# Optimization experiments

Measured on AMD Instinct MI355X. Metric: run time of the kernel, lower is better.

The kernel has to match this reference:

```python
import jax, jax.numpy as jnp
import numpy as np

HEADS = 4
DIM_HEAD = 128


def setup_inputs() -> dict:
    key = jax.random.key(0)
    k1, k2, k3, k4, k5 = jax.random.split(key, 5)
    dim = 256
    f, h, w = 8, 14, 14
    inner = HEADS * DIM_HEAD
    scale = DIM_HEAD ** -0.5
    fmap = jax.random.normal(k1, (8, dim, f, h, w), dtype=jnp.float32)
    # Conv3d 1x1x1, no bias -> plain channel matmul weight [3*inner, dim]
    W_qkv = jax.random.normal(k2, (3 * inner, dim), dtype=jnp.float32) * (dim ** -0.5)
    pos_f = jax.random.normal(k3, (f, DIM_HEAD), dtype=jnp.float32) * scale
    pos_h = jax.random.normal(k4, (h, DIM_HEAD), dtype=jnp.float32) * scale
    pos_w = jax.random.normal(k5, (w, DIM_HEAD), dtype=jnp.float32) * scale
    return {"fmap": fmap, "W_qkv": W_qkv, "pos_f": pos_f, "pos_h": pos_h, "pos_w": pos_w}


def reference(fmap, W_qkv, pos_f, pos_h, pos_w):
    b, c, f, h, w = fmap.shape
    n = f * h * w
    scale = DIM_HEAD ** -0.5
    # 1x1x1 Conv3d == channel matmul
    qkv = jnp.einsum('bcfhw,oc->bofhw', fmap, W_qkv)  # [b, 3*inner, f, h, w]
    q, k, v = jnp.split(qkv, 3, axis=1)
    # 'b (h d) x y z -> b h (x y z) d'
    def to_heads(t):
        return t.reshape(b, HEADS, DIM_HEAD, n).transpose(0, 1, 3, 2)
    q, k, v = to_heads(q), to_heads(k), to_heads(v)
    q = q * scale
    # additive absolute positional embedding [n, d]
    emb = (pos_f[:, None, None, :] + pos_h[None, :, None, :] + pos_w[None, None, :, :]).reshape(n, DIM_HEAD)
    sim = jnp.einsum('bhid,bhjd->bhij', q, k) + jnp.einsum('bhid,jd->bhij', q, emb)
    attn = jax.nn.softmax(sim, axis=-1)
    out = jnp.einsum('bhij,bhjd->bhid', attn, v)  # [b, heads, n, d]
    # 'b h (x y z) d -> b (h d) x y z'
    out = out.transpose(0, 1, 3, 2).reshape(b, HEADS * DIM_HEAD, f, h, w)
    return out
```

## Files before the change

### kernel.cpp

```cpp
#include <hip/hip_runtime.h>
#include <hip/hip_bf16.h>
#include <cstdint>

#define NPOS 1568
#define NQPAD 1664
#define NKVT 25
#define DHEAD 128
#define DIM 256
#define SCALE_Q (0.08838834764831845f * 1.4426950408889634f)

typedef __bf16 bf16x8 __attribute__((ext_vector_type(8)));
typedef float f32x4 __attribute__((ext_vector_type(4)));
typedef float f32x16 __attribute__((ext_vector_type(16)));
typedef unsigned short u16;
typedef u16 u16x8 __attribute__((ext_vector_type(8)));

__device__ __forceinline__ unsigned cvtpk(float a, float b) {
  unsigned r;
  asm("v_cvt_pk_bf16_f32 %0, %1, %2" : "=v"(r) : "v"(a), "v"(b));
  return r;
}

__device__ __forceinline__ void gload_lds16(const void* g, void* s) {
  __builtin_amdgcn_global_load_lds(
      (const __attribute__((address_space(1))) unsigned*)g,
      (__attribute__((address_space(3))) unsigned*)s, 16, 0, 0);
}

__device__ __forceinline__ f32x16 zero16() {
  f32x16 v;
#pragma unroll
  for (int i = 0; i < 16; ++i) v[i] = 0.f;
  return v;
}

__global__ __launch_bounds__(256) void emb_kernel(
    const float* __restrict__ pf, const float* __restrict__ ph,
    const float* __restrict__ pw, float* __restrict__ emb) {
  int idx = blockIdx.x * 256 + threadIdx.x;
  int pos = idx >> 7, d = idx & 127;
  int jf = pos / 196; int r = pos - jf * 196; int jh = r / 14; int jw = r - jh * 14;
  emb[idx] = pf[jf * 128 + d] + ph[jh * 128 + d] + pw[jw * 128 + d];
}

__global__ __launch_bounds__(256) void wconv_kernel(
    const float* __restrict__ W, u16* __restrict__ Wbf) {
  int i8 = (blockIdx.x * 256 + threadIdx.x) * 8;
  float4 f0 = *(const float4*)(W + i8);
  float4 f1 = *(const float4*)(W + i8 + 4);
  union { unsigned u[4]; u16x8 v; } o;
  o.u[0] = cvtpk(f0.x, f0.y); o.u[1] = cvtpk(f0.z, f0.w);
  o.u[2] = cvtpk(f1.x, f1.y); o.u[3] = cvtpk(f1.z, f1.w);
  *(u16x8*)(Wbf + i8) = o.v;
}

__global__ __launch_bounds__(256) void ftrans_kernel(
    const float* __restrict__ fmap, u16* __restrict__ fmapT) {
  __shared__ float t[64][68];
  const int tid = threadIdx.x;
  const int pos0 = blockIdx.x * 64, c0 = blockIdx.y * 64, b = blockIdx.z;
  const int cl = tid >> 3, p8 = (tid & 7) * 8;
  const bool pv = (pos0 + p8) < NPOS;
#pragma unroll
  for (int half = 0; half < 2; ++half) {
    int c = cl + half * 32;
    float4 f0 = {0.f, 0.f, 0.f, 0.f}, f1 = {0.f, 0.f, 0.f, 0.f};
    if (pv) {
      const float* src = fmap + ((size_t)(b * DIM + c0 + c)) * NPOS + pos0 + p8;
      f0 = *(const float4*)src;
      f1 = *(const float4*)(src + 4);
    }
    *(float4*)&t[c][p8] = f0;
    *(float4*)&t[c][p8 + 4] = f1;
  }
  __syncthreads();
  const int pl = tid >> 2, c16 = (tid & 3) * 16;
  const int gpos = pos0 + pl;
  union { unsigned u[8]; } o;
  if (gpos < NPOS) {
#pragma unroll
    for (int i = 0; i < 8; ++i) o.u[i] = cvtpk(t[c16 + 2 * i][pl], t[c16 + 2 * i + 1][pl]);
  } else {
#pragma unroll
    for (int i = 0; i < 8; ++i) o.u[i] = 0;
  }
  u16* dst = fmapT + ((size_t)b * NQPAD + gpos) * DIM + c0 + c16;
  *(uint4*)(dst) = *(uint4*)&o.u[0];
  *(uint4*)(dst + 8) = *(uint4*)&o.u[4];
}

__global__ __launch_bounds__(256, 4) void proj_kernel(
    const u16* __restrict__ Wbf, const u16* __restrict__ fmapT,
    const float* __restrict__ emb, u16* __restrict__ qws, char* __restrict__ tiles) {
  __shared__ float ot[64][132];
  const int tid = threadIdx.x;
  const int lane = tid & 63, w = tid >> 6;
  const int l15 = lane & 15, g = lane >> 4;
  const int wid = blockIdx.x;
  const int b = wid & 7;
  const int gq = wid >> 3;
  const int o0 = (gq / 13) * 128;
  const int pos0 = (gq % 13) * 128;
  const int wo = (w & 1) * 64, wp = (w >> 1) * 64;

  f32x4 acc[4][4];
#pragma unroll
  for (int i = 0; i < 4; ++i)
#pragma unroll
    for (int j = 0; j < 4; ++j) acc[i][j] = (f32x4){0.f, 0.f, 0.f, 0.f};

  const u16* Ab = Wbf + (size_t)(o0 + wo + l15) * DIM + g * 8;
  const u16* Bb = fmapT + ((size_t)b * NQPAD + pos0 + wp + l15) * DIM + g * 8;
#pragma unroll 2
  for (int c0 = 0; c0 < DIM; c0 += 32) {
    bf16x8 a[4], bb[4];
#pragma unroll
    for (int t = 0; t < 4; ++t) a[t] = *(const bf16x8*)(Ab + (size_t)t * 16 * DIM + c0);
#pragma unroll
    for (int t = 0; t < 4; ++t) bb[t] = *(const bf16x8*)(Bb + (size_t)t * 16 * DIM + c0);
#pragma unroll
    for (int i = 0; i < 4; ++i)
#pragma unroll
      for (int j = 0; j < 4; ++j)
        acc[i][j] = __builtin_amdgcn_mfma_f32_16x16x32_bf16(a[i], bb[j], acc[i][j], 0, 0, 0);
  }

  const int sec = o0 >> 9, head = (o0 >> 7) & 3, bh = b * 4 + head;

  if (sec < 2) {
#pragma unroll
    for (int ph = 0; ph < 2; ++ph) {
      __syncthreads();
      if (wp == ph * 64) {
#pragma unroll
        for (int i = 0; i < 4; ++i)
#pragma unroll
          for (int j = 0; j < 4; ++j)
#pragma unroll
            for (int r = 0; r < 4; ++r)
              ot[j * 16 + l15][wo + i * 16 + 4 * g + r] = acc[i][j][r];
      }
      __syncthreads();
      const int pl = tid >> 2, c32 = (tid & 3) * 32;
      const int gpos = pos0 + ph * 64 + pl;
      float v[32];
#pragma unroll
      for (int i = 0; i < 32; ++i) v[i] = ot[pl][c32 + i];
      if (sec == 0) {
#pragma unroll
        for (int q = 0; q < 4; ++q) {
          union { unsigned u[4]; u16x8 h; } o8;
#pragma unroll
          for (int i = 0; i < 4; ++i)
            o8.u[i] = cvtpk(v[q * 8 + 2 * i] * SCALE_Q, v[q * 8 + 2 * i + 1] * SCALE_Q);
          *(u16x8*)(qws + ((size_t)bh * NQPAD + gpos) * DHEAD + c32 + q * 8) = o8.h;
        }
      } else {
        if (gpos < NKVT * 64) {
          if (gpos < NPOS) {
            const float* eb = emb + (size_t)gpos * DHEAD + c32;
#pragma unroll
            for (int i = 0; i < 8; ++i) {
              float4 e = *(const float4*)(eb + i * 4);
              v[i * 4 + 0] += e.x; v[i * 4 + 1] += e.y;
              v[i * 4 + 2] += e.z; v[i * 4 + 3] += e.w;
            }
          }
          const int jt = gpos >> 6, jl = gpos & 63;
          char* base = tiles + ((size_t)(bh * NKVT + jt)) * 32768 + jl * 256;
          const int swz = (jl & 7) << 4;
#pragma unroll
          for (int q = 0; q < 4; ++q) {
            union { unsigned u[4]; u16x8 h; } o8;
#pragma unroll
            for (int i = 0; i < 4; ++i)
              o8.u[i] = cvtpk(v[q * 8 + 2 * i], v[q * 8 + 2 * i + 1]);
            *(u16x8*)(base + (((c32 + q * 8) * 2) ^ swz)) = o8.h;
          }
        }
      }
    }
  } else {
#pragma unroll
    for (int ch = 0; ch < 2; ++ch) {
      __syncthreads();
      if (wo == ch * 64) {
#pragma unroll
        for (int i = 0; i < 4; ++i)
#pragma unroll
          for (int j = 0; j < 4; ++j)
#pragma unroll
            for (int r = 0; r < 4; ++r)
              ot[i * 16 + 4 * g + r][wp + j * 16 + l15] = acc[i][j][r];
      }
      __syncthreads();
      const int dl = tid >> 2, p32 = (tid & 3) * 32;
      const int d = ch * 64 + dl;
      const int gp = pos0 + p32;
      float v[32];
#pragma unroll
      for (int i = 0; i < 32; ++i) v[i] = ot[dl][p32 + i];
      if (gp < NKVT * 64) {
        const int jt = gp >> 6, jl0 = gp & 63;
        char* base = tiles + ((size_t)(bh * NKVT + jt)) * 32768 + 16384 + d * 128;
        const int swz = (d & 7) << 4;
#pragma unroll
        for (int q = 0; q < 4; ++q) {
          union { unsigned u[4]; u16x8 h; } o8;
#pragma unroll
          for (int i = 0; i < 4; ++i)
            o8.u[i] = cvtpk(v[q * 8 + 2 * i], v[q * 8 + 2 * i + 1]);
          *(u16x8*)(base + (((jl0 + q * 8) * 2) ^ swz)) = o8.h;
        }
      }
    }
  }
}

__global__ __launch_bounds__(512, 4) void attn_kernel(
    const u16* __restrict__ qws, const char* __restrict__ tiles,
    float* __restrict__ out) {
  __shared__ char smem[65536];
  const int tid = threadIdx.x;
  const int lane = tid & 63, w = tid >> 6;
  const int qw = w & 3, grp = w >> 2;
  const int l31 = lane & 31, hi = lane >> 5;
  const int wid = blockIdx.x;
  const int bh = (wid & 7) * 4 + (wid >> 3) / 13;
  const int bx = (wid >> 3) % 13;
  const int b = bh >> 2, h = bh & 3;
  const int q0 = bx * 128;
  const int rho = (l31 & 0x13) | ((l31 & 4) << 1) | ((l31 & 8) >> 1);
  const int krow = grp * 32 + rho;
  const int jb = grp * 64;

  bf16x8 qf[8];
  {
    const u16* qp = qws + ((size_t)bh * NQPAD + q0 + qw * 32 + l31) * DHEAD + 8 * hi;
#pragma unroll
    for (int kk = 0; kk < 8; ++kk) qf[kk] = *(const bf16x8*)(qp + kk * 16);
  }

  f32x16 oacc[4];
#pragma unroll
  for (int dt = 0; dt < 4; ++dt) oacc[dt] = zero16();
  float m = -1e30f, l = 0.f;

  const size_t tbase = (size_t)bh * NKVT * 32768;

  {
    const char* src = tiles + tbase + w * 4096 + lane * 16;
    char* dst = smem + w * 4096;
#pragma unroll
    for (int i = 0; i < 4; ++i) gload_lds16(src + i * 1024, dst + i * 1024);
  }
  __syncthreads();

  int cur = 0;
  for (int jt = 0; jt < NKVT; ++jt) {
    if (jt + 1 < NKVT) {
      const char* src = tiles + tbase + (size_t)(jt + 1) * 32768 + w * 4096 + lane * 16;
      char* dst = smem + (cur ^ 1) * 32768 + w * 4096;
#pragma unroll
      for (int i = 0; i < 4; ++i) gload_lds16(src + i * 1024, dst + i * 1024);
    }
    const char* kt = smem + cur * 32768;
    const char* vt = kt + 16384;

    if (grp == 0 || jt < NKVT - 1) {
      f32x16 sc = zero16();
      {
        const int swz = (krow & 7) << 4;
#pragma unroll
        for (int kk = 0; kk < 8; ++kk) {
          bf16x8 ka = *(const bf16x8*)(kt + krow * 256 + ((kk * 32 + 16 * hi) ^ swz));
          sc = __builtin_amdgcn_mfma_f32_32x32x16_bf16(ka, qf[kk], sc, 0, 0, 0);
        }
      }
      float pm = -1e30f;
#pragma unroll
      for (int i = 0; i < 16; ++i) pm = fmaxf(pm, sc[i]);
      pm = fmaxf(pm, __shfl_xor(pm, 32));
      if (!__all(pm <= m + 8.f)) {
        float mn = fmaxf(m, pm);
        float al = exp2f(m - mn);
        m = mn;
        l *= al;
#pragma unroll
        for (int dt = 0; dt < 4; ++dt)
#pragma unroll
          for (int i = 0; i < 16; ++i) oacc[dt][i] *= al;
      }
      float lac = 0.f;
#pragma unroll
      for (int i = 0; i < 16; ++i) { sc[i] = exp2f(sc[i] - m); lac += sc[i]; }
      l += lac;

      union { unsigned u[4]; bf16x8 v; } pb0, pb1;
      pb0.u[0] = cvtpk(sc[0], sc[1]);   pb0.u[1] = cvtpk(sc[2], sc[3]);
      pb0.u[2] = cvtpk(sc[4], sc[5]);   pb0.u[3] = cvtpk(sc[6], sc[7]);
      pb1.u[0] = cvtpk(sc[8], sc[9]);   pb1.u[1] = cvtpk(sc[10], sc[11]);
      pb1.u[2] = cvtpk(sc[12], sc[13]); pb1.u[3] = cvtpk(sc[14], sc[15]);
#pragma unroll
      for (int dt = 0; dt < 4; ++dt) {
        const int row = dt * 32 + l31, swz = (row & 7) << 4;
        bf16x8 va0 = *(const bf16x8*)(vt + row * 128 + ((jb + 16 * hi) ^ swz));
        oacc[dt] = __builtin_amdgcn_mfma_f32_32x32x16_bf16(va0, pb0.v, oacc[dt], 0, 0, 0);
        bf16x8 va1 = *(const bf16x8*)(vt + row * 128 + ((jb + 32 + 16 * hi) ^ swz));
        oacc[dt] = __builtin_amdgcn_mfma_f32_32x32x16_bf16(va1, pb1.v, oacc[dt], 0, 0, 0);
      }
    }
    __syncthreads();
    cur ^= 1;
  }

  float lt = l + __shfl_xor(l, 32);
  float* ml = (float*)smem;
  float* cx = (float*)(smem + 4096);
  if (grp == 1) {
    ml[(qw * 64 + lane) * 2 + 0] = m;
    ml[(qw * 64 + lane) * 2 + 1] = lt;
  }
  __syncthreads();
  float fA = 0.f, fB = 0.f;
  if (grp == 0) {
    float mB = ml[(qw * 64 + lane) * 2 + 0];
    float lB = ml[(qw * 64 + lane) * 2 + 1];
    float ms = fmaxf(m, mB);
    float aA = exp2f(m - ms), aB = exp2f(mB - ms);
    float inv = 1.f / (lt * aA + lB * aB);
    fA = aA * inv; fB = aB * inv;
  }
  const int q = q0 + qw * 32 + l31;
  float* ob = out + (size_t)(b * 512 + h * 128) * NPOS + q;
#pragma unroll
  for (int ch = 0; ch < 2; ++ch) {
    __syncthreads();
    if (grp == 1) {
#pragma unroll
      for (int k = 0; k < 2; ++k)
#pragma unroll
        for (int i = 0; i < 16; ++i)
          cx[(k * 16 + i) * 256 + qw * 64 + lane] = oacc[ch * 2 + k][i];
    }
    __syncthreads();
    if (grp == 0 && q < NPOS) {
#pragma unroll
      for (int k = 0; k < 2; ++k) {
        const int dt = ch * 2 + k;
#pragma unroll
        for (int r = 0; r < 16; ++r) {
          float vB = cx[(k * 16 + r) * 256 + qw * 64 + lane];
          float vo = oacc[dt][r] * fA + vB * fB;
          int d = dt * 32 + (r & 3) + 8 * (r >> 2) + 4 * hi;
          ob[(size_t)d * NPOS] = vo;
        }
      }
    }
  }
}

extern "C" void kernel_launch(void* const* d_in, const int* in_sizes, int n_in,
                              void* d_out, int out_size, void* d_ws, size_t ws_size,
                              hipStream_t stream) {
  const float* fmap = (const float*)d_in[0];
  const float* W    = (const float*)d_in[1];
  const float* pf   = (const float*)d_in[2];
  const float* ph   = (const float*)d_in[3];
  const float* pw   = (const float*)d_in[4];
  float* out = (float*)d_out;

  char* ws = (char*)d_ws;
  const size_t QSZ = (size_t)32 * NQPAD * DHEAD * 2;
  u16* qws    = (u16*)ws;
  char* tiles = ws + QSZ;

  char* oscr = (char*)d_out;
  const size_t FSZ = (size_t)8 * NQPAD * DIM * 2;
  const size_t WSZ = (size_t)1536 * DIM * 2;
  u16* fmapT = (u16*)oscr;
  u16* Wbf   = (u16*)(oscr + FSZ);
  float* emb = (float*)(oscr + FSZ + WSZ);

  emb_kernel<<<dim3(784), dim3(256), 0, stream>>>(pf, ph, pw, emb);
  wconv_kernel<<<dim3(192), dim3(256), 0, stream>>>(W, Wbf);
  ftrans_kernel<<<dim3(26, 4, 8), dim3(256), 0, stream>>>(fmap, fmapT);
  proj_kernel<<<dim3(1248), dim3(256), 0, stream>>>(Wbf, fmapT, emb, qws, tiles);
  attn_kernel<<<dim3(416), dim3(512), 0, stream>>>(qws, tiles, out);
}
```

Baseline: 152.5 us.

## Pre-swizzle K/V tiles into MFMA fragment order and load directly from global

The projection kernel now writes K and V tiles in the exact per-lane MFMA operand layout, so the attention kernel reads fragments straight from global memory (L2) with coalesced 16-byte loads. This drops the LDS double-buffer, global_load_lds staging and the per-tile __syncthreads. The attention kernel shrinks to 256-thread blocks covering 64 queries, doubling the grid. Each wave now fetches its own K/V fragments, so there is no sharing through LDS and global/L2 traffic goes up, and there is no explicit prefetch to hide load latency.

```diff
diff --git a/kernel.cpp b/kernel.cpp
--- a/kernel.cpp
+++ b/kernel.cpp
@@ -19,12 +19,6 @@
   unsigned r;
   asm("v_cvt_pk_bf16_f32 %0, %1, %2" : "=v"(r) : "v"(a), "v"(b));
   return r;
-}
-
-__device__ __forceinline__ void gload_lds16(const void* g, void* s) {
-  __builtin_amdgcn_global_load_lds(
-      (const __attribute__((address_space(1))) unsigned*)g,
-      (__attribute__((address_space(3))) unsigned*)s, 16, 0, 0);
 }
 
 __device__ __forceinline__ f32x16 zero16() {
@@ -167,15 +161,18 @@
             }
           }
           const int jt = gpos >> 6, jl = gpos & 63;
-          char* base = tiles + ((size_t)(bh * NKVT + jt)) * 32768 + jl * 256;
-          const int swz = (jl & 7) << 4;
+          const int grp = jl >> 5, jl31 = jl & 31;
+          const int l31s = (jl31 & 0x13) | ((jl31 & 4) << 1) | ((jl31 & 8) >> 1);
+          char* tb = tiles + ((size_t)(bh * NKVT + jt)) * 32768 + grp * 8192;
 #pragma unroll
           for (int q = 0; q < 4; ++q) {
             union { unsigned u[4]; u16x8 h; } o8;
 #pragma unroll
             for (int i = 0; i < 4; ++i)
               o8.u[i] = cvtpk(v[q * 8 + 2 * i], v[q * 8 + 2 * i + 1]);
-            *(u16x8*)(base + (((c32 + q * 8) * 2) ^ swz)) = o8.h;
+            const int c = c32 + q * 8;
+            const int kk = c >> 4, hi = (c >> 3) & 1;
+            *(u16x8*)(tb + kk * 1024 + (hi * 32 + l31s) * 16) = o8.h;
           }
         }
       }
@@ -202,37 +199,37 @@
       for (int i = 0; i < 32; ++i) v[i] = ot[dl][p32 + i];
       if (gp < NKVT * 64) {
         const int jt = gp >> 6, jl0 = gp & 63;
-        char* base = tiles + ((size_t)(bh * NKVT + jt)) * 32768 + 16384 + d * 128;
-        const int swz = (d & 7) << 4;
+        const int dt = d >> 5, dl31 = d & 31;
+        char* tb = tiles + ((size_t)(bh * NKVT + jt)) * 32768 + 16384;
 #pragma unroll
         for (int q = 0; q < 4; ++q) {
           union { unsigned u[4]; u16x8 h; } o8;
 #pragma unroll
           for (int i = 0; i < 4; ++i)
             o8.u[i] = cvtpk(v[q * 8 + 2 * i], v[q * 8 + 2 * i + 1]);
-          *(u16x8*)(base + (((jl0 + q * 8) * 2) ^ swz)) = o8.h;
+          const int jl = jl0 + q * 8;
+          const int grp = jl >> 5, kj = (jl >> 4) & 1, hi2 = (jl >> 3) & 1;
+          *(u16x8*)(tb + grp * 8192 + dt * 2048 + kj * 1024 + (hi2 * 32 + dl31) * 16) = o8.h;
         }
       }
     }
   }
 }
 
-__global__ __launch_bounds__(512, 4) void attn_kernel(
+__global__ __launch_bounds__(256, 2) void attn_kernel(
     const u16* __restrict__ qws, const char* __restrict__ tiles,
     float* __restrict__ out) {
-  __shared__ char smem[65536];
+  __shared__ float ml[2 * 64 * 2];
+  __shared__ float cx[32 * 128];
   const int tid = threadIdx.x;
   const int lane = tid & 63, w = tid >> 6;
-  const int qw = w & 3, grp = w >> 2;
+  const int qw = w & 1, grp = w >> 1;
   const int l31 = lane & 31, hi = lane >> 5;
   const int wid = blockIdx.x;
-  const int bh = (wid & 7) * 4 + (wid >> 3) / 13;
-  const int bx = (wid >> 3) % 13;
+  const int bh = (wid & 7) * 4 + (wid >> 3) / 26;
+  const int qt = (wid >> 3) % 26;
   const int b = bh >> 2, h = bh & 3;
-  const int q0 = bx * 128;
-  const int rho = (l31 & 0x13) | ((l31 & 4) << 1) | ((l31 & 8) >> 1);
-  const int krow = grp * 32 + rho;
-  const int jb = grp * 64;
+  const int q0 = qt * 64;
 
   bf16x8 qf[8];
   {
@@ -246,37 +243,26 @@
   for (int dt = 0; dt < 4; ++dt) oacc[dt] = zero16();
   float m = -1e30f, l = 0.f;
 
-  const size_t tbase = (size_t)bh * NKVT * 32768;
-
-  {
-    const char* src = tiles + tbase + w * 4096 + lane * 16;
-    char* dst = smem + w * 4096;
-#pragma unroll
-    for (int i = 0; i < 4; ++i) gload_lds16(src + i * 1024, dst + i * 1024);
-  }
-  __syncthreads();
-
-  int cur = 0;
+  const char* kb = tiles + (size_t)bh * NKVT * 32768 + grp * 8192 + lane * 16;
+  const char* vb = kb + 16384;
+
   for (int jt = 0; jt < NKVT; ++jt) {
-    if (jt + 1 < NKVT) {
-      const char* src = tiles + tbase + (size_t)(jt + 1) * 32768 + w * 4096 + lane * 16;
-      char* dst = smem + (cur ^ 1) * 32768 + w * 4096;
-#pragma unroll
-      for (int i = 0; i < 4; ++i) gload_lds16(src + i * 1024, dst + i * 1024);
-    }
-    const char* kt = smem + cur * 32768;
-    const char* vt = kt + 16384;
-
     if (grp == 0 || jt < NKVT - 1) {
+      bf16x8 ka[8];
+#pragma unroll
+      for (int kk = 0; kk < 8; ++kk) ka[kk] = *(const bf16x8*)(kb + kk * 1024);
+      bf16x8 va[4][2];
+#pragma unroll
+      for (int dt = 0; dt < 4; ++dt)
+#pragma unroll
+        for (int kj = 0; kj < 2; ++kj)
+          va[dt][kj] = *(const bf16x8*)(vb + dt * 2048 + kj * 1024);
+
       f32x16 sc = zero16();
-      {
-        const int swz = (krow & 7) << 4;
-#pragma unroll
-        for (int kk = 0; kk < 8; ++kk) {
-          bf16x8 ka = *(const bf16x8*)(kt + krow * 256 + ((kk * 32 + 16 * hi) ^ swz));
-          sc = __builtin_amdgcn_mfma_f32_32x32x16_bf16(ka, qf[kk], sc, 0, 0, 0);
-        }
-      }
+#pragma unroll
+      for (int kk = 0; kk < 8; ++kk)
+        sc = __builtin_amdgcn_mfma_f32_32x32x16_bf16(ka[kk], qf[kk], sc, 0, 0, 0);
+
       float pm = -1e30f;
 #pragma unroll
       for (int i = 0; i < 16; ++i) pm = fmaxf(pm, sc[i]);
@@ -303,20 +289,14 @@
       pb1.u[2] = cvtpk(sc[12], sc[13]); pb1.u[3] = cvtpk(sc[14], sc[15]);
 #pragma unroll
       for (int dt = 0; dt < 4; ++dt) {
-        const int row = dt * 32 + l31, swz = (row & 7) << 4;
-        bf16x8 va0 = *(const bf16x8*)(vt + row * 128 + ((jb + 16 * hi) ^ swz));
-        oacc[dt] = __builtin_amdgcn_mfma_f32_32x32x16_bf16(va0, pb0.v, oacc[dt], 0, 0, 0);
-        bf16x8 va1 = *(const bf16x8*)(vt + row * 128 + ((jb + 32 + 16 * hi) ^ swz));
-        oacc[dt] = __builtin_amdgcn_mfma_f32_32x32x16_bf16(va1, pb1.v, oacc[dt], 0, 0, 0);
-      }
-    }
-    __syncthreads();
-    cur ^= 1;
+        oacc[dt] = __builtin_amdgcn_mfma_f32_32x32x16_bf16(va[dt][0], pb0.v, oacc[dt], 0, 0, 0);
+        oacc[dt] = __builtin_amdgcn_mfma_f32_32x32x16_bf16(va[dt][1], pb1.v, oacc[dt], 0, 0, 0);
+      }
+    }
+    kb += 32768; vb += 32768;
   }
 
   float lt = l + __shfl_xor(l, 32);
-  float* ml = (float*)smem;
-  float* cx = (float*)(smem + 4096);
   if (grp == 1) {
     ml[(qw * 64 + lane) * 2 + 0] = m;
     ml[(qw * 64 + lane) * 2 + 1] = lt;
@@ -341,7 +321,7 @@
       for (int k = 0; k < 2; ++k)
 #pragma unroll
         for (int i = 0; i < 16; ++i)
-          cx[(k * 16 + i) * 256 + qw * 64 + lane] = oacc[ch * 2 + k][i];
+          cx[(k * 16 + i) * 128 + qw * 64 + lane] = oacc[ch * 2 + k][i];
     }
     __syncthreads();
     if (grp == 0 && q < NPOS) {
@@ -350,7 +330,7 @@
         const int dt = ch * 2 + k;
 #pragma unroll
         for (int r = 0; r < 16; ++r) {
-          float vB = cx[(k * 16 + r) * 256 + qw * 64 + lane];
+          float vB = cx[(k * 16 + r) * 128 + qw * 64 + lane];
           float vo = oacc[dt][r] * fA + vB * fB;
           int d = dt * 32 + (r & 3) + 8 * (r >> 2) + 4 * hi;
           ob[(size_t)d * NPOS] = vo;
@@ -386,5 +366,5 @@
   wconv_kernel<<<dim3(192), dim3(256), 0, stream>>>(W, Wbf);
   ftrans_kernel<<<dim3(26, 4, 8), dim3(256), 0, stream>>>(fmap, fmapT);
   proj_kernel<<<dim3(1248), dim3(256), 0, stream>>>(Wbf, fmapT, emb, qws, tiles);
-  attn_kernel<<<dim3(416), dim3(512), 0, stream>>>(qws, tiles, out);
-}
+  attn_kernel<<<dim3(832), dim3(256), 0, stream>>>(qws, tiles, out);
+}
```

New measurement: 145.4 us. 1.05x faster.
